# Optimization experiments

Measured on AMD Instinct MI355X. Metric: run time of the kernel, lower is better.

## Reference

```python
import jax, jax.numpy as jnp
import numpy as np

STRIDE = 2
PAD = 1
K = 4
OUT_PAD = 0


def setup_inputs() -> dict:
    key = jax.random.key(0)
    k1, k2, k3, k4 = jax.random.split(key, 4)
    x = jax.random.normal(k1, (16, 64, 128, 128), dtype=jnp.float32)
    # torch ConvTranspose2d weight layout: [in_channels, out_channels, kH, kW]
    w = jax.random.normal(k2, (64, 32, 4, 4), dtype=jnp.float32) * 0.05
    conv_b = jax.random.normal(k3, (32,), dtype=jnp.float32) * 0.05
    bias = jax.random.normal(k4, (1, 1, 1, 1), dtype=jnp.float32)
    return {"x": x, "w": w, "conv_b": conv_b, "bias": bias}


def conv_transpose2d(x, w, conv_b):
    # Equivalent of torch ConvTranspose2d(k=4, s=2, p=1, op=0):
    # dilate input by stride, pad by k-1-p (+op on trailing side), conv with flipped kernel.
    lo = K - 1 - PAD
    hi = K - 1 - PAD + OUT_PAD
    w_oihw = jnp.flip(w, axis=(2, 3)).transpose(1, 0, 2, 3)  # [Cout, Cin, kH, kW]
    y = jax.lax.conv_general_dilated(
        x, w_oihw,
        window_strides=(1, 1),
        padding=((lo, hi), (lo, hi)),
        lhs_dilation=(STRIDE, STRIDE),
        dimension_numbers=("NCHW", "OIHW", "NCHW"),
    )
    return y + conv_b[None, :, None, None]


def reference(x, w, conv_b, bias):
    y = conv_transpose2d(x, w, conv_b)          # [N, Cout, H', W']
    y = jnp.min(y, axis=1, keepdims=True)       # channel-min -> [N,1,H',W']
    y = jnp.sum(y, axis=2, keepdims=True)       # height-sum  -> [N,1,1,W']
    # kernel uses tanh-based GELU approximation
    return jax.nn.gelu(y, approximate=True) + bias
```

## Files before the change

kernel.cpp:

```cpp
#include <hip/hip_runtime.h>
#include <math.h>

typedef __attribute__((ext_vector_type(8))) short short8;
typedef __attribute__((ext_vector_type(16))) float f32x16;
typedef __attribute__((ext_vector_type(4))) unsigned uintx4;

#define XT_ROWSH 8320
#define XT_NSH   (130 * 8320)
#define XS_ROWB  4352

__device__ __forceinline__ short f2bf(float f) {
    union { float f; unsigned u; } v; v.f = f;
    unsigned r = (v.u + 0x7FFFu + ((v.u >> 16) & 1u)) >> 16;
    return (short)r;
}

__device__ __forceinline__ unsigned cvt_pk_bf16(float lo, float hi) {
    unsigned r;
    asm("v_cvt_pk_bf16_f32 %0, %1, %2" : "=v"(r) : "v"(lo), "v"(hi));
    return r;
}

__device__ __forceinline__ void bar_lds() {
    asm volatile("s_waitcnt lgkmcnt(0)" ::: "memory");
    __builtin_amdgcn_s_barrier();
}

__device__ __forceinline__ void gload_lds16(const void* g, void* l) {
    __builtin_amdgcn_global_load_lds(
        (const __attribute__((address_space(1))) unsigned*)g,
        (__attribute__((address_space(3))) unsigned*)l, 16, 0, 0);
}
__device__ __forceinline__ void gload_lds4(const void* g, void* l) {
    __builtin_amdgcn_global_load_lds(
        (const __attribute__((address_space(1))) unsigned*)g,
        (__attribute__((address_space(3))) unsigned*)l, 4, 0, 0);
}

__global__ void cvt_t(const float* __restrict__ x, const float* __restrict__ w,
                      short* __restrict__ wfrag, short* __restrict__ xt)
{
    int blk = blockIdx.x;
    int t = threadIdx.x;
    if (blk >= 16 * 130) {
        int idx = (blk - 16 * 130) * 256 + t;
        int j    = idx & 7;
        int lane = (idx >> 3) & 63;
        int q    = (idx >> 9) & 15;
        int p    = idx >> 13;
        int co = lane & 31, hf = lane >> 5;
        int ci = (q & 3) * 16 + hf * 8 + j;
        int tq = q >> 2, a = tq >> 1, b = tq & 1;
        int ph = p >> 1, pw = p & 1;
        int kh = 2 * a + 1 - ph, kw = 2 * b + 1 - pw;
        wfrag[idx] = f2bf(w[((ci * 32 + co) * 4 + kh) * 4 + kw]);
        return;
    }
    int n = blk / 130, prow = blk - n * 130;
    short* xr = xt + (size_t)n * XT_NSH + (size_t)prow * XT_ROWSH;

    if (prow == 0 || prow == 129) {
        for (int i = t; i < 1040; i += 256)
            *(uintx4*)(xr + i * 8) = (uintx4)0;
        return;
    }
    if (t < 16) {
        int side = t >> 3, o = t & 7;
        *(uintx4*)(xr + (side ? 129 * 64 : 0) + o * 8) = (uintx4)0;
    }
    int row = prow - 1;
    const float* xb = x + (size_t)n * 64 * 128 * 128 + row * 128;
    int col = t & 31, ci8 = (t >> 5) * 8;
    #pragma unroll
    for (int qd = 0; qd < 4; ++qd) {
        int c0 = col + 32 * qd, pcol = c0 + 1;
        const float* px = xb + (size_t)ci8 * 16384 + c0;
        float v[8];
        #pragma unroll
        for (int c = 0; c < 8; ++c) v[c] = px[(size_t)c * 16384];
        uintx4 u;
        u.x = cvt_pk_bf16(v[0], v[1]); u.y = cvt_pk_bf16(v[2], v[3]);
        u.z = cvt_pk_bf16(v[4], v[5]); u.w = cvt_pk_bf16(v[6], v[7]);
        int off = (ci8 * 2) ^ ((pcol & 7) << 4);
        *(uintx4*)((char*)xr + (size_t)pcol * 128 + off) = u;
    }
}

__global__ __launch_bounds__(256, 3) void convt_mfma(
    const short* __restrict__ xt, const short* __restrict__ wfrag,
    const float* __restrict__ conv_b, float* __restrict__ partials)
{
    __shared__ short xs[10 * 34 * 64];
    __shared__ float minbuf[4][32];

    int blk = ((blockIdx.x & 7) << 7) | (blockIdx.x >> 3);
    const int jq = blk & 3, st = (blk >> 2) & 15, n = blk >> 6;
    const int t  = threadIdx.x;
    const int i0 = st * 8;

    const int wv = t >> 6, lane = t & 63;
    const int ph = wv >> 1, pw = wv & 1;
    const int ln = lane & 31, half = lane >> 5;

    short8 af[16];
    {
        const short8* wf = (const short8*)(wfrag + wv * 8192);
        #pragma unroll
        for (int q = 0; q < 16; ++q) af[q] = wf[q * 64 + lane];
    }
    float cb[16];
    #pragma unroll
    for (int reg = 0; reg < 16; ++reg)
        cb[reg] = conv_b[(reg & 3) + 8 * (reg >> 2) + 4 * half];

    {
        const char* xtn = (const char*)(xt + (size_t)n * XT_NSH);
        for (int r = wv; r < 10; r += 4) {
            const char* src = xtn + (size_t)(i0 + r) * (XT_ROWSH * 2)
                            + (size_t)(jq * 32) * 128;
            char* dst = (char*)xs + r * XS_ROWB;
            #pragma unroll
            for (int ch = 0; ch < 4; ++ch)
                gload_lds16(src + ch * 1024 + lane * 16, dst + ch * 1024);
            gload_lds4(src + 4096 + lane * 4, dst + 4096);
        }
    }
    __syncthreads();

    float osum = 0.f;
    #pragma unroll
    for (int k = 0; k < 4; ++k) {
        const int L0 = 2 * k + ph;
        f32x16 acc0, acc1;
        #pragma unroll
        for (int reg = 0; reg < 16; ++reg) { acc0[reg] = cb[reg]; acc1[reg] = cb[reg]; }
        __builtin_amdgcn_s_setprio(1);
        #pragma unroll
        for (int b = 0; b < 2; ++b) {
            int colp = ln + (pw - b) + 1;
            unsigned swz = (unsigned)(colp & 7) << 4;
            const char* r0 = (const char*)xs + (L0    ) * XS_ROWB + colp * 128;
            const char* r1 = (const char*)xs + (L0 + 1) * XS_ROWB + colp * 128;
            const char* r2 = (const char*)xs + (L0 + 2) * XS_ROWB + colp * 128;
            #pragma unroll
            for (int c = 0; c < 4; ++c) {
                unsigned offp = ((unsigned)(half * 16 + c * 32)) ^ swz;
                short8 Fs = *(const short8*)(r1 + offp);
                acc0 = __builtin_amdgcn_mfma_f32_32x32x16_bf16(af[4*b+c],   Fs, acc0, 0, 0, 0);
                acc1 = __builtin_amdgcn_mfma_f32_32x32x16_bf16(af[8+4*b+c], Fs, acc1, 0, 0, 0);
                short8 F0 = *(const short8*)(r0 + offp);
                acc0 = __builtin_amdgcn_mfma_f32_32x32x16_bf16(af[8+4*b+c], F0, acc0, 0, 0, 0);
                short8 F2 = *(const short8*)(r2 + offp);
                acc1 = __builtin_amdgcn_mfma_f32_32x32x16_bf16(af[4*b+c],   F2, acc1, 0, 0, 0);
            }
        }
        __builtin_amdgcn_s_setprio(0);

        float mn0, mn1;
        {
            float a = fminf(fminf(acc0[0], acc0[1]), fminf(acc0[2], acc0[3]));
            float b2 = fminf(fminf(acc0[4], acc0[5]), fminf(acc0[6], acc0[7]));
            float c = fminf(fminf(acc0[8], acc0[9]), fminf(acc0[10], acc0[11]));
            float d = fminf(fminf(acc0[12], acc0[13]), fminf(acc0[14], acc0[15]));
            mn0 = fminf(fminf(a, b2), fminf(c, d));
            a = fminf(fminf(acc1[0], acc1[1]), fminf(acc1[2], acc1[3]));
            b2 = fminf(fminf(acc1[4], acc1[5]), fminf(acc1[6], acc1[7]));
            c = fminf(fminf(acc1[8], acc1[9]), fminf(acc1[10], acc1[11]));
            d = fminf(fminf(acc1[12], acc1[13]), fminf(acc1[14], acc1[15]));
            mn1 = fminf(fminf(a, b2), fminf(c, d));
        }
        mn0 = fminf(mn0, __shfl_xor(mn0, 32, 64));
        mn1 = fminf(mn1, __shfl_xor(mn1, 32, 64));
        osum += mn0 + mn1;
    }

    if (half == 0) minbuf[wv][ln] = osum;
    bar_lds();

    if (t < 64) {
        int c = t & 31, pwp = t >> 5;
        float v = minbuf[pwp][c] + minbuf[2 + pwp][c];
        int ow = ((jq * 32 + c) << 1) | pwp;
        partials[(size_t)st * 4096 + n * 256 + ow] = v;
    }
}

__global__ void finalize(const float* __restrict__ partials,
                         const float* __restrict__ bias, float* __restrict__ out)
{
    int idx = blockIdx.x * 256 + threadIdx.x;
    float s = 0.f;
    #pragma unroll
    for (int st = 0; st < 16; ++st) s += partials[st * 4096 + idx];
    float u = 0.7978845608028654f * (s + 0.044715f * s * s * s);
    out[idx] = 0.5f * s * (1.f + tanhf(u)) + bias[0];
}

extern "C" void kernel_launch(void* const* d_in, const int* in_sizes, int n_in,
                              void* d_out, int out_size, void* d_ws, size_t ws_size,
                              hipStream_t stream) {
    const float* x      = (const float*)d_in[0];
    const float* w      = (const float*)d_in[1];
    const float* conv_b = (const float*)d_in[2];
    const float* bias   = (const float*)d_in[3];
    float* out = (float*)d_out;

    short* wfrag    = (short*)d_ws;
    float* partials = (float*)((char*)d_ws + 65536);
    short* xt       = (short*)((char*)d_ws + 65536 + 262144);

    hipLaunchKernelGGL(cvt_t, dim3(16 * 130 + 128), dim3(256), 0, stream,
                       x, w, wfrag, xt);
    hipLaunchKernelGGL(convt_mfma, dim3(16 * 16 * 4), dim3(256), 0, stream,
                       xt, wfrag, conv_b, partials);
    hipLaunchKernelGGL(finalize, dim3(16), dim3(256), 0, stream,
                       partials, bias, out);
}
```

Before: 125.6 us.

## Stage input transpose through LDS and fuse finalize via atomics and last-block

The conversion kernel now loads each input row's 64 channels into a swizzled LDS buffer with global_load_lds, then transposes to bf16 from LDS, where before it did strided per-channel global reads. Border-row zeroing moves to separate blocks. The finalize kernel is removed: conv blocks atomically add their partial sums into an accumulator that the prep kernel zeroes, and the last block, found through an atomic counter, applies GELU and bias. This saves one launch and the partials round trip. The cost is atomic contention and a serial tail in a single block.

Result: slower. 130.1 us (+3.5%).

```diff
diff --git a/kernel.cpp b/kernel.cpp
--- a/kernel.cpp
+++ b/kernel.cpp
@@ -38,60 +38,84 @@
 }
 
 __global__ void cvt_t(const float* __restrict__ x, const float* __restrict__ w,
-                      short* __restrict__ wfrag, short* __restrict__ xt)
+                      short* __restrict__ wfrag, short* __restrict__ xt,
+                      float* __restrict__ acc, unsigned* __restrict__ ctr)
 {
     int blk = blockIdx.x;
     int t = threadIdx.x;
-    if (blk >= 16 * 130) {
-        int idx = (blk - 16 * 130) * 256 + t;
-        int j    = idx & 7;
-        int lane = (idx >> 3) & 63;
-        int q    = (idx >> 9) & 15;
-        int p    = idx >> 13;
-        int co = lane & 31, hf = lane >> 5;
-        int ci = (q & 3) * 16 + hf * 8 + j;
-        int tq = q >> 2, a = tq >> 1, b = tq & 1;
-        int ph = p >> 1, pw = p & 1;
-        int kh = 2 * a + 1 - ph, kw = 2 * b + 1 - pw;
-        wfrag[idx] = f2bf(w[((ci * 32 + co) * 4 + kh) * 4 + kw]);
+    if (blk >= 2048) {
+        int e = blk - 2048;
+        if (e < 32) {
+            int n = e >> 1, prow = (e & 1) ? 129 : 0;
+            short* xr = xt + (size_t)n * XT_NSH + (size_t)prow * XT_ROWSH;
+            for (int i = t; i < 1040; i += 256)
+                *(uintx4*)(xr + i * 8) = (uintx4)0;
+        } else if (e < 160) {
+            int idx = (e - 32) * 256 + t;
+            int j    = idx & 7;
+            int lane = (idx >> 3) & 63;
+            int q    = (idx >> 9) & 15;
+            int p    = idx >> 13;
+            int co = lane & 31, hf = lane >> 5;
+            int ci = (q & 3) * 16 + hf * 8 + j;
+            int tq = q >> 2, a = tq >> 1, b = tq & 1;
+            int ph = p >> 1, pw = p & 1;
+            int kh = 2 * a + 1 - ph, kw = 2 * b + 1 - pw;
+            wfrag[idx] = f2bf(w[((ci * 32 + co) * 4 + kh) * 4 + kw]);
+        } else {
+            for (int i = t; i < 4096; i += 256) acc[i] = 0.f;
+            if (t == 0) *ctr = 0u;
+        }
         return;
     }
-    int n = blk / 130, prow = blk - n * 130;
-    short* xr = xt + (size_t)n * XT_NSH + (size_t)prow * XT_ROWSH;
-
-    if (prow == 0 || prow == 129) {
-        for (int i = t; i < 1040; i += 256)
-            *(uintx4*)(xr + i * 8) = (uintx4)0;
-        return;
-    }
+
+    __shared__ float xf[64 * 128];
+    int n = blk >> 7, row = blk & 127;
+    short* xr = xt + (size_t)n * XT_NSH + (size_t)(row + 1) * XT_ROWSH;
+
     if (t < 16) {
         int side = t >> 3, o = t & 7;
         *(uintx4*)(xr + (side ? 129 * 64 : 0) + o * 8) = (uintx4)0;
     }
-    int row = prow - 1;
-    const float* xb = x + (size_t)n * 64 * 128 * 128 + row * 128;
-    int col = t & 31, ci8 = (t >> 5) * 8;
-    #pragma unroll
-    for (int qd = 0; qd < 4; ++qd) {
-        int c0 = col + 32 * qd, pcol = c0 + 1;
-        const float* px = xb + (size_t)ci8 * 16384 + c0;
+
+    const float* xnr = x + (size_t)n * 64 * 16384 + (size_t)row * 128;
+    int wv = t >> 6, lane = t & 63;
+    #pragma unroll
+    for (int i = 0; i < 8; ++i) {
+        int ci0 = wv * 16 + i * 2;
+        int s = (ci0 >> 3) & 7;
+        const float* src = xnr + (size_t)(ci0 + (lane >> 5)) * 16384
+                         + (size_t)(((lane & 31) ^ s) * 4);
+        gload_lds16(src, (char*)xf + ci0 * 512);
+    }
+    __syncthreads();
+
+    #pragma unroll
+    for (int k = 0; k < 4; ++k) {
+        int ch = k * 256 + t;
+        int b = ch & 7, col = ch >> 3, pcol = col + 1;
+        int h = (col >> 2) ^ b;
+        const float* p = xf + (size_t)(b * 8) * 128 + h * 4 + (col & 3);
         float v[8];
         #pragma unroll
-        for (int c = 0; c < 8; ++c) v[c] = px[(size_t)c * 16384];
+        for (int c = 0; c < 8; ++c) v[c] = p[c * 128];
         uintx4 u;
         u.x = cvt_pk_bf16(v[0], v[1]); u.y = cvt_pk_bf16(v[2], v[3]);
         u.z = cvt_pk_bf16(v[4], v[5]); u.w = cvt_pk_bf16(v[6], v[7]);
-        int off = (ci8 * 2) ^ ((pcol & 7) << 4);
-        *(uintx4*)((char*)xr + (size_t)pcol * 128 + off) = u;
+        *(uintx4*)((char*)xr + (size_t)pcol * 128
+                   + ((unsigned)(b * 16) ^ ((unsigned)(pcol & 7) << 4))) = u;
     }
 }
 
 __global__ __launch_bounds__(256, 3) void convt_mfma(
     const short* __restrict__ xt, const short* __restrict__ wfrag,
-    const float* __restrict__ conv_b, float* __restrict__ partials)
+    const float* __restrict__ conv_b, float* __restrict__ acc,
+    unsigned* __restrict__ ctr, const float* __restrict__ bias,
+    float* __restrict__ out)
 {
     __shared__ short xs[10 * 34 * 64];
     __shared__ float minbuf[4][32];
+    __shared__ unsigned lastflag;
 
     int blk = ((blockIdx.x & 7) << 7) | (blockIdx.x >> 3);
     const int jq = blk & 3, st = (blk >> 2) & 15, n = blk >> 6;
@@ -101,6 +125,8 @@
     const int wv = t >> 6, lane = t & 63;
     const int ph = wv >> 1, pw = wv & 1;
     const int ln = lane & 31, half = lane >> 5;
+
+    if (t == 0) lastflag = 0;
 
     short8 af[16];
     {
@@ -181,19 +207,25 @@
         int c = t & 31, pwp = t >> 5;
         float v = minbuf[pwp][c] + minbuf[2 + pwp][c];
         int ow = ((jq * 32 + c) << 1) | pwp;
-        partials[(size_t)st * 4096 + n * 256 + ow] = v;
-    }
-}
-
-__global__ void finalize(const float* __restrict__ partials,
-                         const float* __restrict__ bias, float* __restrict__ out)
-{
-    int idx = blockIdx.x * 256 + threadIdx.x;
-    float s = 0.f;
-    #pragma unroll
-    for (int st = 0; st < 16; ++st) s += partials[st * 4096 + idx];
-    float u = 0.7978845608028654f * (s + 0.044715f * s * s * s);
-    out[idx] = 0.5f * s * (1.f + tanhf(u)) + bias[0];
+        atomicAdd(&acc[n * 256 + ow], v);
+    }
+
+    __syncthreads();
+    if (t == 0) {
+        unsigned old = atomicAdd(ctr, 1u);
+        if (old == 1023u) lastflag = 1;
+    }
+    __syncthreads();
+    if (lastflag) {
+        __threadfence();
+        float b0 = bias[0];
+        for (int i = t; i < 4096; i += 256) {
+            float s = __hip_atomic_load(&acc[i], __ATOMIC_RELAXED,
+                                        __HIP_MEMORY_SCOPE_AGENT);
+            float u = 0.7978845608028654f * (s + 0.044715f * s * s * s);
+            out[i] = 0.5f * s * (1.f + tanhf(u)) + b0;
+        }
+    }
 }
 
 extern "C" void kernel_launch(void* const* d_in, const int* in_sizes, int n_in,
@@ -205,14 +237,13 @@
     const float* bias   = (const float*)d_in[3];
     float* out = (float*)d_out;
 
-    short* wfrag    = (short*)d_ws;
-    float* partials = (float*)((char*)d_ws + 65536);
-    short* xt       = (short*)((char*)d_ws + 65536 + 262144);
-
-    hipLaunchKernelGGL(cvt_t, dim3(16 * 130 + 128), dim3(256), 0, stream,
-                       x, w, wfrag, xt);
+    short*    wfrag = (short*)d_ws;
+    float*    acc   = (float*)((char*)d_ws + 65536);
+    unsigned* ctr   = (unsigned*)((char*)d_ws + 81920);
+    short*    xt    = (short*)((char*)d_ws + 98304);
+
+    hipLaunchKernelGGL(cvt_t, dim3(2048 + 32 + 128 + 1), dim3(256), 0, stream,
+                       x, w, wfrag, xt, acc, ctr);
     hipLaunchKernelGGL(convt_mfma, dim3(16 * 16 * 4), dim3(256), 0, stream,
-                       xt, wfrag, conv_b, partials);
-    hipLaunchKernelGGL(finalize, dim3(16), dim3(256), 0, stream,
-                       partials, bias, out);
-}
+                       xt, wfrag, conv_b, acc, ctr, bias, out);
+}
```
